# Optimization experiments

Hardware: AMD Instinct MI355X
Metric: run time of the kernel (lower is better)

Reference implementation:

```python
import jax, jax.numpy as jnp
import numpy as np

B, JX, JQ, D = 16, 4096, 512, 256
VERY_NEG = -1e30


def setup_inputs() -> dict:
    key = jax.random.key(0)
    ks = jax.random.split(key, 8)
    c = jax.random.normal(ks[0], (B, JX, D), dtype=jnp.float32)
    q = jax.random.normal(ks[1], (B, JQ, D), dtype=jnp.float32)
    # glorot-ish scaled weights for [4d, d] projections
    s = 1.0 / np.sqrt(4 * D)
    Wr = jax.random.normal(ks[2], (4 * D, D), dtype=jnp.float32) * s
    Wg = jax.random.normal(ks[3], (4 * D, D), dtype=jnp.float32) * s
    Br = jnp.zeros((D,), dtype=jnp.float32)
    Bg = jnp.zeros((D,), dtype=jnp.float32)
    # padding masks from random valid lengths (realistic ragged batch)
    c_len = jax.random.randint(ks[4], (B,), JX // 2, JX + 1)
    q_len = jax.random.randint(ks[5], (B,), JQ // 2, JQ + 1)
    c_mask = jnp.arange(JX)[None, :] < c_len[:, None]
    q_mask = jnp.arange(JQ)[None, :] < q_len[:, None]
    return {"c": c, "q": q, "Wr": Wr, "Br": Br, "Wg": Wg, "Bg": Bg,
            "c_mask": c_mask, "q_mask": q_mask}


def reference(c, q, Wr, Br, Wg, Bg, c_mask, q_mask):
    # logits[b,x,j] = <c[b,x], q[b,j]>
    logits = jnp.einsum('bxd,bjd->bxj', c, q)
    # exp_mask: add VERY_NEG where (c_mask & q_mask) is False
    cq_mask = c_mask[:, :, None] & q_mask[:, None, :]  # [B,JX,JQ]
    logits = logits + (1.0 - cq_mask.astype(logits.dtype)) * VERY_NEG
    a = jax.nn.softmax(logits, axis=-1)                # [B,JX,JQ]
    q_a = jnp.einsum('bxj,bjd->bxd', a, q)             # [B,JX,D]
    # semantic fusion unit
    cc = jnp.concatenate([c, q_a, c * q_a, c - q_a], axis=-1)  # [B,JX,4D]
    r_ = jnp.tanh(cc @ Wr + Br)
    g = jax.nn.sigmoid(cc @ Wg + Bg)
    return g * r_ + (1.0 - g) * c
```

## Files before the change

### kernel.cpp

```cpp
#include <hip/hip_runtime.h>
#include <hip/hip_bf16.h>
#include <stdint.h>

#define NB 16
#define JXX 4096
#define JQQ 512
#define DDD 256
#define LOG2E 1.44269504f

typedef __attribute__((ext_vector_type(8))) _Float16 f16x8;
typedef __attribute__((ext_vector_type(4))) _Float16 f16x4;
typedef __attribute__((ext_vector_type(4))) float f32x4;

__device__ __forceinline__ uint16_t f2h(float f) {
    union { _Float16 h; uint16_t s; } u; u.h = (_Float16)f; return u.s;
}
__device__ __forceinline__ float h2f(uint16_t s) {
    union { _Float16 h; uint16_t s; } u; u.s = s; return (float)u.h;
}

__device__ __forceinline__ void gload_lds16(const void* g, void* l) {
    __builtin_amdgcn_global_load_lds(
        (const __attribute__((address_space(1))) void*)g,
        (__attribute__((address_space(3))) void*)l, 16, 0, 0);
}

#define VMW(N) asm volatile("s_waitcnt vmcnt(" #N ")" ::: "memory")

__global__ void k_mask(const void* cmask, const void* qmask,
                       uint8_t* cm8, uint8_t* qm8) {
    int i = blockIdx.x * 256 + threadIdx.x;
    uint32_t w0c = *(const uint32_t*)cmask;
    uint32_t w0q = *(const uint32_t*)qmask;
    int mc = (w0c == 1u) ? 1 : (w0c == 0x3f800000u ? 2 : 0);
    int mq = (w0q == 1u) ? 1 : (w0q == 0x3f800000u ? 2 : 0);
    if (i < NB * JXX) {
        uint8_t v;
        if (mc == 1)      v = ((const int*)cmask)[i] != 0;
        else if (mc == 2) v = ((const float*)cmask)[i] != 0.0f;
        else              v = ((const uint8_t*)cmask)[i] != 0;
        cm8[i] = v;
    }
    if (i < NB * JQQ) {
        uint8_t v;
        if (mq == 1)      v = ((const int*)qmask)[i] != 0;
        else if (mq == 2) v = ((const float*)qmask)[i] != 0.0f;
        else              v = ((const uint8_t*)qmask)[i] != 0;
        qm8[i] = v;
    }
}

__global__ void k_prep_q(const float* __restrict__ qg,
                         uint16_t* __restrict__ qS,
                         uint16_t* __restrict__ qTS) {
    __shared__ float tile[64][65];
    const int b = blockIdx.z, j0 = blockIdx.x * 64, d0 = blockIdx.y * 64;
    const int t = threadIdx.x;
    #pragma unroll
    for (int i = 0; i < 16; i++) {
        int e = t + 256 * i;
        int r = e >> 6, c = e & 63;
        tile[r][c] = qg[((long)b * JQQ + j0 + r) * DDD + d0 + c];
    }
    __syncthreads();
    #pragma unroll
    for (int i = 0; i < 2; i++) {
        int e = t + 256 * i;
        int r = e >> 3, c8 = e & 7;
        f16x8 v;
        #pragma unroll
        for (int k = 0; k < 8; k++) v[k] = (_Float16)tile[r][c8 * 8 + k];
        int jt = (j0 >> 5) + (r >> 5);
        int row = r & 31;
        int d8 = (d0 >> 3) + c8;
        int byt = ((row * 512 + d8 * 16) ^ ((row & 7) << 4));
        *(f16x8*)(qS + ((long)(b * 16 + jt)) * 8192 + (byt >> 1)) = v;
    }
    #pragma unroll
    for (int i = 0; i < 2; i++) {
        int e = t + 256 * i;
        int dd = e >> 3, j8 = e & 7;
        f16x8 v;
        #pragma unroll
        for (int k = 0; k < 8; k++) v[k] = (_Float16)tile[j8 * 8 + k][dd];
        int jt = (j0 >> 5) + (j8 >> 2);
        int d = d0 + dd;
        int byt = ((d * 64 + (j8 & 3) * 16) ^ (((d >> 1) & 3) << 4));
        *(f16x8*)(qTS + ((long)(b * 16 + jt)) * 8192 + (byt >> 1)) = v;
    }
}

__global__ void k_prep_w(const float* __restrict__ Wr, const float* __restrict__ Wg,
                         uint16_t* __restrict__ WP2) {
    __shared__ _Float16 tile[32 * 264];
    const int rg = blockIdx.y;
    const float* W = rg ? Wg : Wr;
    const int kt = blockIdx.x, t = threadIdx.x;
    #pragma unroll
    for (int i = 0; i < 32; i++) {
        int e = t + 256 * i;
        int r = e >> 8, c = e & 255;
        tile[r * 264 + c] = (_Float16)W[(long)(kt * 32 + r) * 256 + c];
    }
    __syncthreads();
    const int step = (kt & 7) * 4 + (kt >> 3);
    #pragma unroll
    for (int ss = 0; ss < 4; ss++) {
        int slot = ss * 256 + t;
        int ntg = slot >> 6, lane = slot & 63;
        int gg = lane >> 4, l = lane & 15;
        f16x8 v;
        #pragma unroll
        for (int i = 0; i < 8; i++) v[i] = tile[(gg * 8 + i) * 264 + ntg * 16 + l];
        int hh = ntg >> 3, ntl = ntg & 7;
        long off = (long)step * 16384 + hh * 8192 + rg * 4096 + ntl * 512 + lane * 8;
        *(f16x8*)(WP2 + off) = v;
    }
}

__global__ __launch_bounds__(256, 2) void k_attn(
    const float* __restrict__ cg,
    const uint16_t* __restrict__ qS,
    const uint16_t* __restrict__ qTS,
    const uint8_t* __restrict__ cm8,
    const uint8_t* __restrict__ qm8,
    uint16_t* __restrict__ qa16,
    uint16_t* __restrict__ c16)
{
    __shared__ __align__(16) uint16_t qbuf[2][8192];
    __shared__ __align__(16) uint16_t qTbuf[2][8192];
    __shared__ __align__(16) uint16_t P_lds[4 * 32 * 40];
    __shared__ __align__(16) uint32_t qm_lds[128];

    const int b = blockIdx.y;
    const int t = threadIdx.x;
    const int wave = t >> 6;
    const int lane = t & 63;
    const int l15 = lane & 15;
    const int g = lane >> 4;
    const int xw = blockIdx.x * 128 + wave * 32;

    if (t < 128) {
        uint32_t m = ((const uint32_t*)(qm8 + (long)b * JQQ))[t];
        qm_lds[t] = m;
    }

    f16x8 cfrag[2][8];
    bool cvalid[2];
    float m_run[2], s_run[2];
    #pragma unroll
    for (int xs = 0; xs < 2; xs++) {
        const long rowg = (long)b * JXX + xw + xs * 16 + l15;
        const float* crow = cg + rowg * DDD;
        uint16_t* c16row = c16 + rowg * DDD;
        #pragma unroll
        for (int kb = 0; kb < 8; kb++) {
            float4 v0 = *(const float4*)(crow + kb * 32 + g * 8);
            float4 v1 = *(const float4*)(crow + kb * 32 + g * 8 + 4);
            f16x8 f;
            f[0] = (_Float16)v0.x; f[1] = (_Float16)v0.y; f[2] = (_Float16)v0.z; f[3] = (_Float16)v0.w;
            f[4] = (_Float16)v1.x; f[5] = (_Float16)v1.y; f[6] = (_Float16)v1.z; f[7] = (_Float16)v1.w;
            cfrag[xs][kb] = f;
            *(f16x8*)(c16row + kb * 32 + g * 8) = f;
        }
        cvalid[xs] = cm8[rowg] != 0;
        m_run[xs] = cvalid[xs] ? -1e30f : 0.0f;
        s_run[xs] = 0.0f;
    }
    const f32x4 fzero = {0.f, 0.f, 0.f, 0.f};
    f32x4 qa[16][2];
    #pragma unroll
    for (int i = 0; i < 16; i++) { qa[i][0] = fzero; qa[i][1] = fzero; }

    const uint16_t* qSb  = qS  + (long)(b * 16) * 8192;
    const uint16_t* qTSb = qTS + (long)(b * 16) * 8192;

    const int kbit = (l15 >> 2) & 1;
    const int qbase = l15 * 256 + (((g * 16) ^ ((l15 & 3) << 4)) >> 1);
    const int qTbase = l15 * 32 + ((g ^ ((l15 >> 1) & 3)) * 8);

    #define STAGE_ATTN(bsel, tile)                                              \
        {                                                                       \
            const uint16_t* s1 = qSb + (long)(tile) * 8192;                     \
            const uint16_t* s2 = qTSb + (long)(tile) * 8192;                    \
            _Pragma("unroll")                                                   \
            for (int i = 0; i < 4; i++)                                         \
                gload_lds16(s1 + i * 2048 + t * 8,                              \
                            &qbuf[bsel][i * 2048 + wave * 512]);                \
            _Pragma("unroll")                                                   \
            for (int i = 0; i < 4; i++)                                         \
                gload_lds16(s2 + i * 2048 + t * 8,                              \
                            &qTbuf[bsel][i * 2048 + wave * 512]);               \
        }

    STAGE_ATTN(0, 0);
    asm volatile("s_waitcnt lgkmcnt(0)" ::: "memory");
    __builtin_amdgcn_s_barrier();

    int cur = 0;
    for (int jt = 0; jt < 16; jt++) {
        if (jt < 15) {
            STAGE_ATTN(cur ^ 1, jt + 1);
            VMW(8);
        } else {
            VMW(0);
        }
        __builtin_amdgcn_s_barrier();
        __builtin_amdgcn_sched_barrier(0);

        const uint16_t* qb_l  = &qbuf[cur][0];
        const uint16_t* qTb_l = &qTbuf[cur][0];

        uint32_t qmw[2];
        qmw[0] = qm_lds[jt * 8 + g];
        qmw[1] = qm_lds[jt * 8 + 4 + g];

        f32x4 acc[2][2];
        acc[0][0] = fzero; acc[0][1] = fzero; acc[1][0] = fzero; acc[1][1] = fzero;
        #pragma unroll
        for (int js = 0; js < 2; js++) {
            #pragma unroll
            for (int kb = 0; kb < 8; kb++) {
                f16x8 qf = *(const f16x8*)(qb_l + js * 4096 + qbase + ((kb ^ kbit) << 5));
                acc[js][0] = __builtin_amdgcn_mfma_f32_16x16x32_f16(qf, cfrag[0][kb], acc[js][0], 0, 0, 0);
                acc[js][1] = __builtin_amdgcn_mfma_f32_16x16x32_f16(qf, cfrag[1][kb], acc[js][1], 0, 0, 0);
            }
        }

        f16x4 pv[2][2];
        float fsc[2];
        #pragma unroll
        for (int xs = 0; xs < 2; xs++) {
            float lmax = -1e30f;
            #pragma unroll
            for (int js = 0; js < 2; js++) {
                #pragma unroll
                for (int r = 0; r < 4; r++) {
                    bool qv = (qmw[js] >> (8 * r)) & 0xffu;
                    lmax = fmaxf(lmax, qv ? acc[js][xs][r] : -1e30f);
                }
            }
            lmax = fmaxf(lmax, __shfl_xor(lmax, 16));
            lmax = fmaxf(lmax, __shfl_xor(lmax, 32));
            float m_new = cvalid[xs] ? fmaxf(m_run[xs], lmax) : 0.0f;
            fsc[xs] = exp2f((m_run[xs] - m_new) * LOG2E);
            float psum = 0.0f;
            #pragma unroll
            for (int js = 0; js < 2; js++) {
                #pragma unroll
                for (int r = 0; r < 4; r++) {
                    bool qv = (qmw[js] >> (8 * r)) & 0xffu;
                    float p = qv ? exp2f((acc[js][xs][r] - m_new) * LOG2E) : 0.0f;
                    if (!cvalid[xs]) p = 1.0f;
                    psum += p;
                    pv[xs][js][r] = (_Float16)p;
                }
            }
            s_run[xs] = s_run[xs] * fsc[xs] + psum;
            m_run[xs] = m_new;
        }
        if (!__all(fsc[0] == 1.0f && fsc[1] == 1.0f)) {
            #pragma unroll
            for (int dt = 0; dt < 16; dt++) {
                #pragma unroll
                for (int xs = 0; xs < 2; xs++) {
                    qa[dt][xs][0] *= fsc[xs]; qa[dt][xs][1] *= fsc[xs];
                    qa[dt][xs][2] *= fsc[xs]; qa[dt][xs][3] *= fsc[xs];
                }
            }
        }

        uint16_t* Pw0 = P_lds + wave * 1280;
        #pragma unroll
        for (int xs = 0; xs < 2; xs++) {
            *(f16x4*)(Pw0 + (xs * 16 + l15) * 40 + g * 4) = pv[xs][0];
            *(f16x4*)(Pw0 + (xs * 16 + l15) * 40 + 16 + g * 4) = pv[xs][1];
        }
        f16x8 pa[2];
        pa[0] = *(const f16x8*)(Pw0 + l15 * 40 + g * 8);
        pa[1] = *(const f16x8*)(Pw0 + (16 + l15) * 40 + g * 8);

        #pragma unroll
        for (int dt = 0; dt < 16; dt++) {
            f16x8 bq = *(const f16x8*)(qTb_l + qTbase + dt * 512);
            qa[dt][0] = __builtin_amdgcn_mfma_f32_16x16x32_f16(bq, pa[0], qa[dt][0], 0, 0, 0);
            qa[dt][1] = __builtin_amdgcn_mfma_f32_16x16x32_f16(bq, pa[1], qa[dt][1], 0, 0, 0);
        }

        __builtin_amdgcn_sched_barrier(0);
        __builtin_amdgcn_s_barrier();
        cur ^= 1;
    }
    #undef STAGE_ATTN

    #pragma unroll
    for (int xs = 0; xs < 2; xs++) {
        float s_tot = s_run[xs] + __shfl_xor(s_run[xs], 16);
        s_tot = s_tot + __shfl_xor(s_tot, 32);
        float inv = 1.0f / s_tot;
        uint16_t* outp = qa16 + ((long)b * JXX + xw + xs * 16 + l15) * DDD;
        #pragma unroll
        for (int dt = 0; dt < 16; dt++) {
            f16x4 v;
            v[0] = (_Float16)(qa[dt][xs][0] * inv);
            v[1] = (_Float16)(qa[dt][xs][1] * inv);
            v[2] = (_Float16)(qa[dt][xs][2] * inv);
            v[3] = (_Float16)(qa[dt][xs][3] * inv);
            *(f16x4*)(outp + dt * 16 + g * 4) = v;
        }
    }
}

__global__ __launch_bounds__(256, 2) void k_sfu(
    const uint16_t* __restrict__ c16g,
    const uint16_t* __restrict__ qa16,
    const uint16_t* __restrict__ WP2,
    const float* __restrict__ Brb,
    const float* __restrict__ Bgb,
    float* __restrict__ outg)
{
    __shared__ __align__(16) uint16_t ab_lds[2][4096];
    __shared__ __align__(16) uint16_t wbuf[3][8192];

    const int t = threadIdx.x;
    const int wave = t >> 6, lane = t & 63;
    const int l15 = lane & 15, g = lane >> 4;
    const int nw = wave;
    const long m0 = (long)blockIdx.x * 64;
    const int h = blockIdx.y, n0 = h * 128;

    const uint16_t* WPh = WP2 + (long)h * 8192;

    const f32x4 fzero = {0.f, 0.f, 0.f, 0.f};
    f32x4 accR[4][2], accG[4][2];
    #pragma unroll
    for (int a = 0; a < 4; a++)
        #pragma unroll
        for (int bq = 0; bq < 2; bq++) { accR[a][bq] = fzero; accG[a][bq] = fzero; }

    #define STAGE_CQA(dt_)                                                        \
        { _Pragma("unroll")                                                       \
          for (int j = 0; j < 2; j++) {                                           \
              int pp = j * 256 + t;                                               \
              int row = pp >> 3, pc = pp & 7;                                     \
              long src = (m0 + row) * 256 + (dt_) * 64 + ((pc ^ (row & 7)) << 3); \
              int dst = (j * 256 + wave * 64) * 8;                                \
              gload_lds16(c16g + src, &ab_lds[0][dst]);                           \
              gload_lds16(qa16 + src, &ab_lds[1][dst]);                           \
          } }

    #define STAGE_W(s_)                                                           \
        { _Pragma("unroll")                                                       \
          for (int i = 0; i < 4; i++)                                             \
              gload_lds16(WPh + (long)(s_) * 16384 + i * 2048 + wave * 512 + lane * 8, \
                          &wbuf[(s_) % 3][i * 2048 + wave * 512]); }

    STAGE_CQA(0);
    STAGE_W(0);
    STAGE_W(1);
    VMW(8);
    __builtin_amdgcn_s_barrier();

    #pragma unroll
    for (int dt = 0; dt < 4; dt++) {
        #pragma unroll
        for (int kb = 0; kb < 2; kb++) {
            f16x8 af[4][4];
            #pragma unroll
            for (int mf = 0; mf < 4; mf++) {
                int row = mf * 16 + l15;
                int c8 = kb * 4 + g;
                int off = row * 64 + ((c8 ^ (row & 7)) << 3);
                f16x8 cf = *(const f16x8*)(&ab_lds[0][off]);
                f16x8 qf = *(const f16x8*)(&ab_lds[1][off]);
                af[0][mf] = cf;
                af[1][mf] = qf;
                af[2][mf] = cf * qf;
                af[3][mf] = cf - qf;
            }
            #pragma unroll
            for (int comp = 0; comp < 4; comp++) {
                const int s = dt * 8 + kb * 4 + comp;
                if (s <= 29) STAGE_W(s + 2);
                if (dt < 3 && kb == 1 && comp == 1) STAGE_CQA(dt + 1);
                if (s == 31)      { VMW(0); }
                else if (s == 30) { VMW(4); }
                else if (dt < 3 && kb == 1 && (comp == 1 || comp == 2)) { VMW(12); }
                else              { VMW(8); }
                __builtin_amdgcn_s_barrier();
                __builtin_amdgcn_sched_barrier(0);
                const uint16_t* Wb = &wbuf[s % 3][nw * 1024 + lane * 8];
                #pragma unroll
                for (int nt = 0; nt < 2; nt++) {
                    f16x8 br = *(const f16x8*)(Wb + nt * 512);
                    f16x8 bg = *(const f16x8*)(Wb + 4096 + nt * 512);
                    #pragma unroll
                    for (int mf = 0; mf < 4; mf++) {
                        accR[mf][nt] = __builtin_amdgcn_mfma_f32_16x16x32_f16(af[comp][mf], br, accR[mf][nt], 0, 0, 0);
                        accG[mf][nt] = __builtin_amdgcn_mfma_f32_16x16x32_f16(af[comp][mf], bg, accG[mf][nt], 0, 0, 0);
                    }
                }
                __builtin_amdgcn_sched_barrier(0);
                __builtin_amdgcn_s_barrier();
            }
        }
    }
    #undef STAGE_W
    #undef STAGE_CQA

    #pragma unroll
    for (int nt = 0; nt < 2; nt++) {
        int n = n0 + nw * 32 + nt * 16 + l15;
        float br = Brb[n], bg = Bgb[n];
        #pragma unroll
        for (int mf = 0; mf < 4; mf++) {
            long rowb = m0 + mf * 16 + g * 4;
            #pragma unroll
            for (int r = 0; r < 4; r++) {
                float pr = accR[mf][nt][r] + br;
                float pg = accG[mf][nt][r] + bg;
                float x = fminf(fmaxf(pr, -30.f), 30.f);
                float e2 = __expf(2.f * x);
                float rr = (e2 - 1.f) / (e2 + 1.f);
                float gv = 1.0f / (1.0f + __expf(-pg));
                float cv = h2f(c16g[(rowb + r) * DDD + n]);
                outg[(rowb + r) * DDD + n] = gv * rr + (1.f - gv) * cv;
            }
        }
    }
}

extern "C" void kernel_launch(void* const* d_in, const int* in_sizes, int n_in,
                              void* d_out, int out_size, void* d_ws, size_t ws_size,
                              hipStream_t stream) {
    const float* c  = (const float*)d_in[0];
    const float* q  = (const float*)d_in[1];
    const float* Wr = (const float*)d_in[2];
    const float* Br = (const float*)d_in[3];
    const float* Wg = (const float*)d_in[4];
    const float* Bg = (const float*)d_in[5];
    const void* cmask = d_in[6];
    const void* qmask = d_in[7];

    char* ws = (char*)d_ws;
    uint16_t* qS    = (uint16_t*)(ws + 0);
    uint16_t* qTS   = (uint16_t*)(ws + 4194304);
    uint16_t* qa16  = (uint16_t*)(ws + 8388608);
    uint16_t* c16   = (uint16_t*)(ws + 41943040);
    uint16_t* WP2   = (uint16_t*)(ws + 75497472);
    uint8_t*  cm8   = (uint8_t*)(ws + 77594624);
    uint8_t*  qm8   = (uint8_t*)(ws + 77660160);
    (void)in_sizes; (void)n_in; (void)out_size; (void)ws_size;

    k_mask<<<dim3((NB * JXX + 255) / 256), dim3(256), 0, stream>>>(cmask, qmask, cm8, qm8);
    k_prep_q<<<dim3(8, 4, NB), dim3(256), 0, stream>>>(q, qS, qTS);
    k_prep_w<<<dim3(32, 2), dim3(256), 0, stream>>>(Wr, Wg, WP2);
    k_attn<<<dim3(JXX / 128, NB), dim3(256), 0, stream>>>(c, qS, qTS, cm8, qm8, qa16, c16);
    k_sfu<<<dim3((NB * JXX) / 64, 2), dim3(256), 0, stream>>>(
        c16, qa16, WP2, Br, Bg, (float*)d_out);
}
```

Measured before the change: 169.1 us.

## Load SFU weights directly into registers and double-buffer c/q_a tiles in LDS

The fused-unit GEMM kernel no longer stages the pre-packed weight slices through a triple-buffered LDS ring. Each lane now reads its weight fragments straight from global memory into registers, prefetching one step ahead into a ping-pong pair. The c/q_a activation tiles move to a double-buffered LDS layout, so the per-step barriers and vmcnt waits shrink to one __syncthreads per d-tile. This cuts LDS traffic and synchronisation, but the MFMAs now depend on global (L2) latency for weights, which a single step of prefetch may not fully hide.

```diff
diff --git a/kernel.cpp b/kernel.cpp
--- a/kernel.cpp
+++ b/kernel.cpp
@@ -319,8 +319,7 @@
     const float* __restrict__ Bgb,
     float* __restrict__ outg)
 {
-    __shared__ __align__(16) uint16_t ab_lds[2][4096];
-    __shared__ __align__(16) uint16_t wbuf[3][8192];
+    __shared__ __align__(16) uint16_t ab_lds[2][2][4096];
 
     const int t = threadIdx.x;
     const int wave = t >> 6, lane = t & 63;
@@ -329,7 +328,7 @@
     const long m0 = (long)blockIdx.x * 64;
     const int h = blockIdx.y, n0 = h * 128;
 
-    const uint16_t* WPh = WP2 + (long)h * 8192;
+    const uint16_t* wbase = WP2 + (long)h * 8192 + nw * 1024 + lane * 8;
 
     const f32x4 fzero = {0.f, 0.f, 0.f, 0.f};
     f32x4 accR[4][2], accG[4][2];
@@ -338,75 +337,71 @@
         #pragma unroll
         for (int bq = 0; bq < 2; bq++) { accR[a][bq] = fzero; accG[a][bq] = fzero; }
 
-    #define STAGE_CQA(dt_)                                                        \
+    #define STAGE_CQA(dt_, nb_)                                                   \
         { _Pragma("unroll")                                                       \
           for (int j = 0; j < 2; j++) {                                           \
               int pp = j * 256 + t;                                               \
               int row = pp >> 3, pc = pp & 7;                                     \
               long src = (m0 + row) * 256 + (dt_) * 64 + ((pc ^ (row & 7)) << 3); \
               int dst = (j * 256 + wave * 64) * 8;                                \
-              gload_lds16(c16g + src, &ab_lds[0][dst]);                           \
-              gload_lds16(qa16 + src, &ab_lds[1][dst]);                           \
+              gload_lds16(c16g + src, &ab_lds[nb_][0][dst]);                      \
+              gload_lds16(qa16 + src, &ab_lds[nb_][1][dst]);                      \
           } }
 
-    #define STAGE_W(s_)                                                           \
-        { _Pragma("unroll")                                                       \
-          for (int i = 0; i < 4; i++)                                             \
-              gload_lds16(WPh + (long)(s_) * 16384 + i * 2048 + wave * 512 + lane * 8, \
-                          &wbuf[(s_) % 3][i * 2048 + wave * 512]); }
-
-    STAGE_CQA(0);
-    STAGE_W(0);
-    STAGE_W(1);
-    VMW(8);
-    __builtin_amdgcn_s_barrier();
+    #define LOAD_W(dst, s_)                                                       \
+        { dst[0] = *(const f16x8*)(wbase + (long)(s_) * 16384);                   \
+          dst[1] = *(const f16x8*)(wbase + (long)(s_) * 16384 + 512);             \
+          dst[2] = *(const f16x8*)(wbase + (long)(s_) * 16384 + 4096);            \
+          dst[3] = *(const f16x8*)(wbase + (long)(s_) * 16384 + 4608); }
+
+    f16x8 wA[4], wB[4];
+    STAGE_CQA(0, 0);
+    LOAD_W(wA, 0);
+    __syncthreads();
 
     #pragma unroll
     for (int dt = 0; dt < 4; dt++) {
         #pragma unroll
         for (int kb = 0; kb < 2; kb++) {
-            f16x8 af[4][4];
+            f16x8 cfr[4], qfr[4];
             #pragma unroll
             for (int mf = 0; mf < 4; mf++) {
                 int row = mf * 16 + l15;
                 int c8 = kb * 4 + g;
                 int off = row * 64 + ((c8 ^ (row & 7)) << 3);
-                f16x8 cf = *(const f16x8*)(&ab_lds[0][off]);
-                f16x8 qf = *(const f16x8*)(&ab_lds[1][off]);
-                af[0][mf] = cf;
-                af[1][mf] = qf;
-                af[2][mf] = cf * qf;
-                af[3][mf] = cf - qf;
+                cfr[mf] = *(const f16x8*)(&ab_lds[dt & 1][0][off]);
+                qfr[mf] = *(const f16x8*)(&ab_lds[dt & 1][1][off]);
             }
             #pragma unroll
             for (int comp = 0; comp < 4; comp++) {
                 const int s = dt * 8 + kb * 4 + comp;
-                if (s <= 29) STAGE_W(s + 2);
-                if (dt < 3 && kb == 1 && comp == 1) STAGE_CQA(dt + 1);
-                if (s == 31)      { VMW(0); }
-                else if (s == 30) { VMW(4); }
-                else if (dt < 3 && kb == 1 && (comp == 1 || comp == 2)) { VMW(12); }
-                else              { VMW(8); }
-                __builtin_amdgcn_s_barrier();
-                __builtin_amdgcn_sched_barrier(0);
-                const uint16_t* Wb = &wbuf[s % 3][nw * 1024 + lane * 8];
+                f16x8 (&wc)[4] = (s & 1) ? wB : wA;
+                f16x8 (&wn)[4] = (s & 1) ? wA : wB;
+                if (s < 31) LOAD_W(wn, s + 1);
+                if (dt < 3 && kb == 1 && comp == 2) STAGE_CQA(dt + 1, (dt + 1) & 1);
+                f16x8 afc[4];
+                #pragma unroll
+                for (int mf = 0; mf < 4; mf++) {
+                    if (comp == 0)      afc[mf] = cfr[mf];
+                    else if (comp == 1) afc[mf] = qfr[mf];
+                    else if (comp == 2) afc[mf] = cfr[mf] * qfr[mf];
+                    else                afc[mf] = cfr[mf] - qfr[mf];
+                }
                 #pragma unroll
                 for (int nt = 0; nt < 2; nt++) {
-                    f16x8 br = *(const f16x8*)(Wb + nt * 512);
-                    f16x8 bg = *(const f16x8*)(Wb + 4096 + nt * 512);
+                    f16x8 br = wc[nt], bg = wc[2 + nt];
                     #pragma unroll
                     for (int mf = 0; mf < 4; mf++) {
-                        accR[mf][nt] = __builtin_amdgcn_mfma_f32_16x16x32_f16(af[comp][mf], br, accR[mf][nt], 0, 0, 0);
-                        accG[mf][nt] = __builtin_amdgcn_mfma_f32_16x16x32_f16(af[comp][mf], bg, accG[mf][nt], 0, 0, 0);
+                        accR[mf][nt] = __builtin_amdgcn_mfma_f32_16x16x32_f16(afc[mf], br, accR[mf][nt], 0, 0, 0);
+                        accG[mf][nt] = __builtin_amdgcn_mfma_f32_16x16x32_f16(afc[mf], bg, accG[mf][nt], 0, 0, 0);
                     }
                 }
-                __builtin_amdgcn_sched_barrier(0);
-                __builtin_amdgcn_s_barrier();
-            }
-        }
-    }
-    #undef STAGE_W
+            }
+        }
+        if (dt < 3) __syncthreads();
+    }
     #undef STAGE_CQA
+    #undef LOAD_W
 
     #pragma unroll
     for (int nt = 0; nt < 2; nt++) {
```

After: 182.7 us. 8.0% more time.

## Compute all 256 output columns per SFU block and double-buffer weights

Applied to the files above, without the earlier changes.

The SFU GEMM block now covers the full N=256 output width instead of splitting it across two blocks, so the concatenated activation tile (c, q_a, c*q_a, c-q_a) is loaded and built once rather than twice. Weight staging changes from triple-buffered 128-column slices to double-buffered full-width slices, and the derived activation fragments are computed per component just before use. Each wave now holds twice as many accumulators and each block issues twice the weight traffic per step, which raises register pressure and halves the grid size, possibly hurting occupancy and latency hiding with only two weight buffers.

```diff
diff --git a/kernel.cpp b/kernel.cpp
--- a/kernel.cpp
+++ b/kernel.cpp
@@ -320,23 +320,21 @@
     float* __restrict__ outg)
 {
     __shared__ __align__(16) uint16_t ab_lds[2][4096];
-    __shared__ __align__(16) uint16_t wbuf[3][8192];
+    __shared__ __align__(16) uint16_t wbuf[2][16384];
 
     const int t = threadIdx.x;
     const int wave = t >> 6, lane = t & 63;
     const int l15 = lane & 15, g = lane >> 4;
-    const int nw = wave;
     const long m0 = (long)blockIdx.x * 64;
-    const int h = blockIdx.y, n0 = h * 128;
-
-    const uint16_t* WPh = WP2 + (long)h * 8192;
 
     const f32x4 fzero = {0.f, 0.f, 0.f, 0.f};
-    f32x4 accR[4][2], accG[4][2];
+    f32x4 accR[4][4], accG[4][4];
     #pragma unroll
     for (int a = 0; a < 4; a++)
         #pragma unroll
-        for (int bq = 0; bq < 2; bq++) { accR[a][bq] = fzero; accG[a][bq] = fzero; }
+        for (int bq = 0; bq < 4; bq++) { accR[a][bq] = fzero; accG[a][bq] = fzero; }
+
+    const int wrd = (wave >> 1) * 8192 + (wave & 1) * 2048 + lane * 8;
 
     #define STAGE_CQA(dt_)                                                        \
         { _Pragma("unroll")                                                       \
@@ -351,53 +349,56 @@
 
     #define STAGE_W(s_)                                                           \
         { _Pragma("unroll")                                                       \
-          for (int i = 0; i < 4; i++)                                             \
-              gload_lds16(WPh + (long)(s_) * 16384 + i * 2048 + wave * 512 + lane * 8, \
-                          &wbuf[(s_) % 3][i * 2048 + wave * 512]); }
+          for (int i = 0; i < 8; i++)                                             \
+              gload_lds16(WP2 + (long)(s_) * 16384 + i * 2048 + t * 8,            \
+                          &wbuf[(s_) & 1][i * 2048 + wave * 512]); }
 
     STAGE_CQA(0);
     STAGE_W(0);
-    STAGE_W(1);
-    VMW(8);
+    VMW(0);
     __builtin_amdgcn_s_barrier();
+    __builtin_amdgcn_sched_barrier(0);
 
     #pragma unroll
     for (int dt = 0; dt < 4; dt++) {
         #pragma unroll
         for (int kb = 0; kb < 2; kb++) {
-            f16x8 af[4][4];
+            f16x8 cfr[4], qfr[4];
             #pragma unroll
             for (int mf = 0; mf < 4; mf++) {
                 int row = mf * 16 + l15;
                 int c8 = kb * 4 + g;
                 int off = row * 64 + ((c8 ^ (row & 7)) << 3);
-                f16x8 cf = *(const f16x8*)(&ab_lds[0][off]);
-                f16x8 qf = *(const f16x8*)(&ab_lds[1][off]);
-                af[0][mf] = cf;
-                af[1][mf] = qf;
-                af[2][mf] = cf * qf;
-                af[3][mf] = cf - qf;
+                cfr[mf] = *(const f16x8*)(&ab_lds[0][off]);
+                qfr[mf] = *(const f16x8*)(&ab_lds[1][off]);
             }
             #pragma unroll
             for (int comp = 0; comp < 4; comp++) {
                 const int s = dt * 8 + kb * 4 + comp;
-                if (s <= 29) STAGE_W(s + 2);
+                if (s < 31) STAGE_W(s + 1);
                 if (dt < 3 && kb == 1 && comp == 1) STAGE_CQA(dt + 1);
-                if (s == 31)      { VMW(0); }
-                else if (s == 30) { VMW(4); }
+                if (s == 31)                                   { VMW(0); }
                 else if (dt < 3 && kb == 1 && (comp == 1 || comp == 2)) { VMW(12); }
-                else              { VMW(8); }
+                else                                           { VMW(8); }
                 __builtin_amdgcn_s_barrier();
                 __builtin_amdgcn_sched_barrier(0);
-                const uint16_t* Wb = &wbuf[s % 3][nw * 1024 + lane * 8];
+                f16x8 afc[4];
                 #pragma unroll
-                for (int nt = 0; nt < 2; nt++) {
+                for (int mf = 0; mf < 4; mf++) {
+                    if (comp == 0)      afc[mf] = cfr[mf];
+                    else if (comp == 1) afc[mf] = qfr[mf];
+                    else if (comp == 2) afc[mf] = cfr[mf] * qfr[mf];
+                    else                afc[mf] = cfr[mf] - qfr[mf];
+                }
+                const uint16_t* Wb = &wbuf[s & 1][wrd];
+                #pragma unroll
+                for (int nt = 0; nt < 4; nt++) {
                     f16x8 br = *(const f16x8*)(Wb + nt * 512);
                     f16x8 bg = *(const f16x8*)(Wb + 4096 + nt * 512);
                     #pragma unroll
                     for (int mf = 0; mf < 4; mf++) {
-                        accR[mf][nt] = __builtin_amdgcn_mfma_f32_16x16x32_f16(af[comp][mf], br, accR[mf][nt], 0, 0, 0);
-                        accG[mf][nt] = __builtin_amdgcn_mfma_f32_16x16x32_f16(af[comp][mf], bg, accG[mf][nt], 0, 0, 0);
+                        accR[mf][nt] = __builtin_amdgcn_mfma_f32_16x16x32_f16(afc[mf], br, accR[mf][nt], 0, 0, 0);
+                        accG[mf][nt] = __builtin_amdgcn_mfma_f32_16x16x32_f16(afc[mf], bg, accG[mf][nt], 0, 0, 0);
                     }
                 }
                 __builtin_amdgcn_sched_barrier(0);
@@ -409,8 +410,8 @@
     #undef STAGE_CQA
 
     #pragma unroll
-    for (int nt = 0; nt < 2; nt++) {
-        int n = n0 + nw * 32 + nt * 16 + l15;
+    for (int nt = 0; nt < 4; nt++) {
+        int n = wave * 64 + nt * 16 + l15;
         float br = Brb[n], bg = Bgb[n];
         #pragma unroll
         for (int mf = 0; mf < 4; mf++) {
@@ -456,6 +457,6 @@
     k_prep_q<<<dim3(8, 4, NB), dim3(256), 0, stream>>>(q, qS, qTS);
     k_prep_w<<<dim3(32, 2), dim3(256), 0, stream>>>(Wr, Wg, WP2);
     k_attn<<<dim3(JXX / 128, NB), dim3(256), 0, stream>>>(c, qS, qTS, cm8, qm8, qa16, c16);
-    k_sfu<<<dim3((NB * JXX) / 64, 2), dim3(256), 0, stream>>>(
+    k_sfu<<<dim3((NB * JXX) / 64), dim3(256), 0, stream>>>(
         c16, qa16, WP2, Br, Bg, (float*)d_out);
 }
```

After: 163.6 us. 3.3% less time.
